# Optimization experiments

Measured on AMD Instinct MI355X. Metric: run time of the kernel, lower is better.

Reference implementation:

```python
import jax, jax.numpy as jnp
import numpy as np

T, B, M = 512, 4096, 2
DT = 1.0
HARD_RESET = True


def setup_inputs() -> dict:
    key = jax.random.key(0)
    ks = jax.random.split(key, 8)
    x_seq = jax.random.normal(ks[0], (T, B), jnp.float32) * 0.5
    w = jax.random.normal(ks[1], (B, B), jnp.float32) * (0.5 / np.sqrt(B))
    b = jax.random.normal(ks[2], (B,), jnp.float32) * 0.1
    v0 = jnp.zeros((B,), jnp.float32)
    Iasc0 = jnp.zeros((B, M), jnp.float32)
    v_th = jnp.ones((B,), jnp.float32)
    v_reset = jnp.zeros((B,), jnp.float32)
    v_rest = jnp.zeros((B,), jnp.float32)
    c_m = jnp.ones((B,), jnp.float32)
    tau = jax.random.uniform(ks[3], (B,), jnp.float32, 5.0, 20.0)
    k = jax.random.uniform(ks[4], (B, M), jnp.float32, 0.1, 0.5)
    asc = jax.random.normal(ks[5], (B, M), jnp.float32) * 0.1
    mask = jnp.ones((B,), jnp.float32)
    return dict(x_seq=x_seq, w=w, b=b, v0=v0, Iasc0=Iasc0, v_th=v_th,
                v_reset=v_reset, v_rest=v_rest, c_m=c_m, tau=tau, k=k,
                asc=asc, mask=mask)


def reference(x_seq, w, b, v0, Iasc0, v_th, v_reset, v_rest, c_m, tau, k, asc, mask):
    a = jnp.exp(-DT / tau)                 # (B,) voltage decay
    bdec = jnp.exp(-k * DT)                # (B,M) ASC decay

    def step(carry, x_t):
        v, I, s_prev = carry
        I_sum = I.sum(-1)                  # (B,)
        lin = w @ s_prev                   # recurrent GEMV against prev spikes
        x = x_t + b + lin
        v_inf = v_rest + tau * (x + I_sum) / c_m
        v_p = v_inf + (v - v_inf) * a
        u = (v_p - v_th) / (v_th - v_reset)
        s = (u > 0.0).astype(v_p.dtype) * mask
        if HARD_RESET:
            v_post = v_p - (v_p - v_reset) * s
        else:
            v_post = v_p - (v_th - v_reset) * s
        I_new = I * bdec + asc * s[:, None]
        return (v_post, I_new, s), (s, v_post)

    (v_fin, I_fin, _), (s_seq, v_seq) = jax.lax.scan(
        step, (v0, Iasc0, jnp.zeros_like(v0)), x_seq)
    return s_seq, v_seq, v_fin, I_fin
```

## Files before the change

### kernel.cpp

```cpp
#include <hip/hip_runtime.h>
#include <math.h>

#define TSTEPS 512
#define BN 4096
#define NBLK 64
#define NTHR 576
#define NPB 64
#define NGW 8
#define ESTRIDE 16

typedef unsigned long long u64;

__device__ __forceinline__ u64 ld_agent(const u64* p) {
    return __hip_atomic_load(p, __ATOMIC_RELAXED, __HIP_MEMORY_SCOPE_AGENT);
}
__device__ __forceinline__ void pub_agent(u64* p, u64 v) {
    (void)__hip_atomic_exchange(p, v, __ATOMIC_RELAXED, __HIP_MEMORY_SCOPE_AGENT);
}
__device__ __forceinline__ void st_flag(unsigned* p, unsigned v) {
    __hip_atomic_store(p, v, __ATOMIC_RELEASE, __HIP_MEMORY_SCOPE_WORKGROUP);
}
__device__ __forceinline__ unsigned ld_flag(const unsigned* p) {
    return __hip_atomic_load(p, __ATOMIC_ACQUIRE, __HIP_MEMORY_SCOPE_WORKGROUP);
}

template<bool TR>
__global__ __launch_bounds__(NTHR, 1)
void glif_kernel(const float* __restrict__ x_seq, const float* __restrict__ w,
                 const float* __restrict__ b_in, const float* __restrict__ v0,
                 const float* __restrict__ Ia0, const float* __restrict__ vth_in,
                 const float* __restrict__ vrst_in, const float* __restrict__ vrest_in,
                 const float* __restrict__ cm_in, const float* __restrict__ tau_in,
                 const float* __restrict__ k_in, const float* __restrict__ asc_in,
                 const float* __restrict__ mask_in,
                 float* __restrict__ out_s, float* __restrict__ out_v,
                 float* __restrict__ out_vf, float* __restrict__ out_if,
                 u64* __restrict__ sbuf, unsigned* __restrict__ bar,
                 float* __restrict__ wT)
{
    __shared__ float    tile[64][65];
    __shared__ int      wlist[NGW][512];
    __shared__ float4   partials[4][NGW][16];
    __shared__ unsigned flags[NGW];

    const int blk = blockIdx.x;
    const int tid = threadIdx.x;
    const int n0 = blk * NPB;
    const int wv = tid >> 6;
    const int ln = tid & 63;

    if (TR) {
        for (int tt = 0; tt < 64; ++tt) {
            int tile_id = blk + tt * NBLK;
            int ti = tile_id >> 6, tj = tile_id & 63;
            if (tid < 512) {
                int c = tid & 63, r0 = tid >> 6;
#pragma unroll
                for (int rr = 0; rr < 8; ++rr) {
                    int r = r0 + rr * 8;
                    tile[r][c] = w[(size_t)(ti * 64 + r) * BN + tj * 64 + c];
                }
            }
            __syncthreads();
            if (tid < 512) {
                int rw = tid & 63, c0 = tid >> 6;
#pragma unroll
                for (int cc = 0; cc < 8; ++cc) {
                    int cw = c0 + cc * 8;
                    float mcol = mask_in[tj * 64 + cw];
                    wT[(size_t)(tj * 64 + cw) * BN + ti * 64 + rw] = tile[rw][cw] * mcol;
                }
            }
            __syncthreads();
        }
    }

    if (tid < NGW) flags[tid] = 0;

    __syncthreads();
    if (tid == 0) {
        __threadfence();
        __hip_atomic_fetch_add(bar, 1u, __ATOMIC_ACQ_REL, __HIP_MEMORY_SCOPE_AGENT);
        while (__hip_atomic_load(bar, __ATOMIC_RELAXED, __HIP_MEMORY_SCOPE_AGENT) < NBLK) {
            __builtin_amdgcn_s_sleep(8);
        }
        __threadfence();
    }
    __syncthreads();

    if (wv == 0) {
        const int n = n0 + ln;
        float v, I0, I1, bb, aa, bd0, bd1, as0, as1, vth, vrst, vrest, cm, tau, msk;
        v = v0[n]; I0 = Ia0[2 * n]; I1 = Ia0[2 * n + 1];
        bb = b_in[n]; vth = vth_in[n]; vrst = vrst_in[n]; vrest = vrest_in[n];
        cm = cm_in[n]; tau = tau_in[n]; msk = mask_in[n];
        aa  = (float)exp((double)(-1.0f / tau));
        bd0 = (float)exp((double)(-k_in[2 * n]));
        bd1 = (float)exp((double)(-k_in[2 * n + 1]));
        as0 = asc_in[2 * n]; as1 = asc_in[2 * n + 1];

        for (int t = 0; t < TSTEPS; ++t) {
            float xt = x_seq[(size_t)t * BN + n];

            {
                const unsigned want = (unsigned)(t + 1);
                const unsigned* fp = &flags[ln & 7];
                while (ld_flag(fp) < want) {}
            }
            const float* pf = reinterpret_cast<const float*>(&partials[t & 3][0][0]);
            float l0 = pf[ln],        l1 = pf[64 + ln],  l2 = pf[128 + ln], l3 = pf[192 + ln];
            float l4 = pf[256 + ln],  l5 = pf[320 + ln], l6 = pf[384 + ln], l7 = pf[448 + ln];
            float lin = ((l0 + l1) + (l2 + l3)) + ((l4 + l5) + (l6 + l7));
            float xx = (xt + bb) + lin;
            float Isum = I0 + I1;
            float vinf = vrest + (tau * (xx + Isum)) / cm;
            float vp = vinf + (v - vinf) * aa;
            float uu = (vp - vth) / (vth - vrst);
            float s = (uu > 0.0f) ? msk : 0.0f;
            u64 bal = __ballot(s != 0.0f);
            u64 tagw = ((u64)(t + 1)) << 32;
            u64* dst = sbuf + ((size_t)((t + 1) & 1) * NBLK + blk) * ESTRIDE;
            if (ln < 2) pub_agent(dst + ln, tagw | (u64)(unsigned)(bal >> (32 * ln)));
            float vpost = vp - (vp - vrst) * s;
            I0 = I0 * bd0 + as0 * s;
            I1 = I1 * bd1 + as1 * s;
            v = vpost;
            out_s[(size_t)t * BN + n] = s;
            out_v[(size_t)t * BN + n] = vpost;
        }
        out_vf[n] = v;
        out_if[2 * n] = I0;
        out_if[2 * n + 1] = I1;
    } else {
        const int gw = wv - 1;
        const int e = ln >> 3;
        const int sub = ln & 7;
        const int wsel = sub >> 2;
        const int bshift = 8 * (sub & 3);
        const int entry = gw * 8 + e;
        const int cbase = (entry << 6) + (sub << 3);
        const int cslot = ln >> 4, l16 = ln & 15;
        const float* wb4 = wT + n0 + l16 * 4;

        for (int t = 0; t < TSTEPS; ++t) {
            const u64* p = sbuf + ((size_t)(t & 1) * NBLK + entry) * ESTRIDE + wsel;
            const unsigned want = (unsigned)t;
            u64 ev;
            for (;;) {
                u64 A = ld_agent(p);
                u64 B = ld_agent(p);
                if ((unsigned)(A >> 32) == want) { ev = A; break; }
                if ((unsigned)(B >> 32) == want) { ev = B; break; }
            }
            unsigned byte = ((unsigned)ev >> bshift) & 0xFFu;

            int c = __popc(byte);
            int x = c;
#pragma unroll
            for (int d = 1; d < 64; d <<= 1) {
                int y = __shfl_up(x, d);
                if (ln >= d) x += y;
            }
            const int kw = __shfl(x, 63);
            int base = x - c;
            while (byte) { int bp = __ffs(byte) - 1; byte &= byte - 1; wlist[gw][base++] = cbase + bp; }

            if (TR) {
                float4 acc = make_float4(0.f, 0.f, 0.f, 0.f);
                const int R = (kw + 3) >> 2;
                for (int r = 0; r < R; r += 8) {
#pragma unroll
                    for (int u = 0; u < 8; ++u) {
                        int idx = (r + u) * 4 + cslot;
                        bool pg = idx < kw;
                        int j = wlist[gw][pg ? idx : 0];
                        float m = pg ? 1.0f : 0.0f;
                        const float4 wvv = *reinterpret_cast<const float4*>(wb4 + ((size_t)j << 12));
                        acc.x = fmaf(wvv.x, m, acc.x);
                        acc.y = fmaf(wvv.y, m, acc.y);
                        acc.z = fmaf(wvv.z, m, acc.z);
                        acc.w = fmaf(wvv.w, m, acc.w);
                    }
                }
#pragma unroll
                for (int d = 16; d < 64; d <<= 1) {
                    acc.x += __shfl_xor(acc.x, d);
                    acc.y += __shfl_xor(acc.y, d);
                    acc.z += __shfl_xor(acc.z, d);
                    acc.w += __shfl_xor(acc.w, d);
                }
                if (ln < 16) partials[t & 3][gw][ln] = acc;
            } else {
                float accs = 0.f;
                const float* wrow = w + (size_t)(n0 + ln) * BN;
                for (int i = 0; i < kw; ++i) {
                    int j = wlist[gw][i];
                    accs = fmaf(wrow[j], mask_in[j], accs);
                }
                reinterpret_cast<float*>(&partials[t & 3][gw][0])[ln] = accs;
            }
            if (ln == 0) st_flag(&flags[gw], (unsigned)(t + 1));
        }
    }
}

extern "C" void kernel_launch(void* const* d_in, const int* in_sizes, int n_in,
                              void* d_out, int out_size, void* d_ws, size_t ws_size,
                              hipStream_t stream)
{
    const float* x_seq = (const float*)d_in[0];
    const float* w     = (const float*)d_in[1];
    const float* b     = (const float*)d_in[2];
    const float* v0    = (const float*)d_in[3];
    const float* Ia0   = (const float*)d_in[4];
    const float* vth   = (const float*)d_in[5];
    const float* vrst  = (const float*)d_in[6];
    const float* vrest = (const float*)d_in[7];
    const float* cm    = (const float*)d_in[8];
    const float* tau   = (const float*)d_in[9];
    const float* k     = (const float*)d_in[10];
    const float* asc   = (const float*)d_in[11];
    const float* mask  = (const float*)d_in[12];

    float* out_s  = (float*)d_out;
    float* out_v  = out_s + (size_t)TSTEPS * BN;
    float* out_vf = out_v + (size_t)TSTEPS * BN;
    float* out_if = out_vf + BN;

    const size_t mb_bytes = (size_t)2 * NBLK * ESTRIDE * sizeof(u64);
    u64* sbuf     = (u64*)d_ws;
    unsigned* bar = (unsigned*)((char*)d_ws + mb_bytes);
    float* wT     = (float*)((char*)d_ws + mb_bytes + 256);

    const size_t need = mb_bytes + 256 + (size_t)BN * BN * sizeof(float);
    const bool tr = (ws_size >= need);

    hipMemsetAsync(d_ws, 0, mb_bytes + 256, stream);

    if (tr) {
        glif_kernel<true><<<NBLK, NTHR, 0, stream>>>(
            x_seq, w, b, v0, Ia0, vth, vrst, vrest, cm, tau, k, asc, mask,
            out_s, out_v, out_vf, out_if, sbuf, bar, wT);
    } else {
        glif_kernel<false><<<NBLK, NTHR, 0, stream>>>(
            x_seq, w, b, v0, Ia0, vth, vrst, vrest, cm, tau, k, asc, mask,
            out_s, out_v, out_vf, out_if, sbuf, bar, (float*)w);
    }
}
```

Before: 1.664 ms.

## Replicate neuron state across 8 block groups and poll spike mailboxes via L2

Launches 256 blocks arranged as 8 replicas of 32 ranks, each rank owning 128 neurons. Every replica redundantly computes the full network state, so spike exchange stays within a replica group, presumably to keep mailbox traffic local to one XCD. Mailboxes are written both with a plain store and an agent-scope store, and readers poll an sc0 global load with a periodic agent-scope fallback. This trades 8x redundant GEMV and weight reads, plus a reliance on non-coherent L2 polling semantics, for lower cross-die synchronisation latency per timestep.

```diff
diff --git a/kernel.cpp b/kernel.cpp
--- a/kernel.cpp
+++ b/kernel.cpp
@@ -3,19 +3,31 @@
 
 #define TSTEPS 512
 #define BN 4096
-#define NBLK 64
+#define NBLK 256
 #define NTHR 576
-#define NPB 64
+#define NPB 128
+#define NREP 8
+#define BPR 32
+#define NWREP 128
 #define NGW 8
-#define ESTRIDE 16
+#define WPW 16
 
 typedef unsigned long long u64;
 
+__device__ __forceinline__ u64 ld_l2(const u64* p) {
+    u64 v;
+    asm volatile("global_load_dwordx2 %0, %1, off sc0\n\ts_waitcnt vmcnt(0)"
+                 : "=v"(v) : "v"(p) : "memory");
+    return v;
+}
+__device__ __forceinline__ void st_l2(u64* p, u64 v) {
+    asm volatile("global_store_dwordx2 %0, %1, off" :: "v"(p), "v"(v) : "memory");
+}
 __device__ __forceinline__ u64 ld_agent(const u64* p) {
     return __hip_atomic_load(p, __ATOMIC_RELAXED, __HIP_MEMORY_SCOPE_AGENT);
 }
-__device__ __forceinline__ void pub_agent(u64* p, u64 v) {
-    (void)__hip_atomic_exchange(p, v, __ATOMIC_RELAXED, __HIP_MEMORY_SCOPE_AGENT);
+__device__ __forceinline__ void st_agent(u64* p, u64 v) {
+    __hip_atomic_store(p, v, __ATOMIC_RELAXED, __HIP_MEMORY_SCOPE_AGENT);
 }
 __device__ __forceinline__ void st_flag(unsigned* p, unsigned v) {
     __hip_atomic_store(p, v, __ATOMIC_RELEASE, __HIP_MEMORY_SCOPE_WORKGROUP);
@@ -35,22 +47,24 @@
                  const float* __restrict__ mask_in,
                  float* __restrict__ out_s, float* __restrict__ out_v,
                  float* __restrict__ out_vf, float* __restrict__ out_if,
-                 u64* __restrict__ sbuf, unsigned* __restrict__ bar,
-                 float* __restrict__ wT)
+                 u64* __restrict__ fastmb, u64* __restrict__ fbmb,
+                 unsigned* __restrict__ bar, float* __restrict__ wT)
 {
     __shared__ float    tile[64][65];
     __shared__ int      wlist[NGW][512];
-    __shared__ float4   partials[4][NGW][16];
+    __shared__ float4   part4[4][NGW][32];
     __shared__ unsigned flags[NGW];
 
     const int blk = blockIdx.x;
     const int tid = threadIdx.x;
-    const int n0 = blk * NPB;
     const int wv = tid >> 6;
     const int ln = tid & 63;
+    const int rep = blk & 7;
+    const int rank = blk >> 3;
+    const int n0 = rank * NPB;
 
     if (TR) {
-        for (int tt = 0; tt < 64; ++tt) {
+        for (int tt = 0; tt < 16; ++tt) {
             int tile_id = blk + tt * NBLK;
             int ti = tile_id >> 6, tj = tile_id & 63;
             if (tid < 512) {
@@ -88,71 +102,110 @@
     }
     __syncthreads();
 
+    u64* fastP = fastmb + (size_t)rep * 2 * NWREP;
+    u64* fbP   = fbmb   + (size_t)rep * 2 * NWREP;
+
     if (wv == 0) {
-        const int n = n0 + ln;
-        float v, I0, I1, bb, aa, bd0, bd1, as0, as1, vth, vrst, vrest, cm, tau, msk;
-        v = v0[n]; I0 = Ia0[2 * n]; I1 = Ia0[2 * n + 1];
-        bb = b_in[n]; vth = vth_in[n]; vrst = vrst_in[n]; vrest = vrest_in[n];
-        cm = cm_in[n]; tau = tau_in[n]; msk = mask_in[n];
-        aa  = (float)exp((double)(-1.0f / tau));
-        bd0 = (float)exp((double)(-k_in[2 * n]));
-        bd1 = (float)exp((double)(-k_in[2 * n + 1]));
-        as0 = asc_in[2 * n]; as1 = asc_in[2 * n + 1];
+        const int nlo = n0 + ln, nhi = n0 + 64 + ln;
+        float vA = v0[nlo], vB = v0[nhi];
+        float I0A = Ia0[2 * nlo], I1A = Ia0[2 * nlo + 1];
+        float I0B = Ia0[2 * nhi], I1B = Ia0[2 * nhi + 1];
+        float bbA = b_in[nlo], bbB = b_in[nhi];
+        float vthA = vth_in[nlo], vthB = vth_in[nhi];
+        float vrA = vrst_in[nlo], vrB = vrst_in[nhi];
+        float veA = vrest_in[nlo], veB = vrest_in[nhi];
+        float cmA = cm_in[nlo], cmB = cm_in[nhi];
+        float tauA = tau_in[nlo], tauB = tau_in[nhi];
+        float mkA = mask_in[nlo], mkB = mask_in[nhi];
+        float aaA = (float)exp((double)(-1.0f / tauA));
+        float aaB = (float)exp((double)(-1.0f / tauB));
+        float b0A = (float)exp((double)(-k_in[2 * nlo]));
+        float b1A = (float)exp((double)(-k_in[2 * nlo + 1]));
+        float b0B = (float)exp((double)(-k_in[2 * nhi]));
+        float b1B = (float)exp((double)(-k_in[2 * nhi + 1]));
+        float s0A = asc_in[2 * nlo], s1A = asc_in[2 * nlo + 1];
+        float s0B = asc_in[2 * nhi], s1B = asc_in[2 * nhi + 1];
 
         for (int t = 0; t < TSTEPS; ++t) {
-            float xt = x_seq[(size_t)t * BN + n];
+            float xlo = x_seq[(size_t)t * BN + nlo];
+            float xhi = x_seq[(size_t)t * BN + nhi];
 
             {
                 const unsigned want = (unsigned)(t + 1);
                 const unsigned* fp = &flags[ln & 7];
                 while (ld_flag(fp) < want) {}
             }
-            const float* pf = reinterpret_cast<const float*>(&partials[t & 3][0][0]);
-            float l0 = pf[ln],        l1 = pf[64 + ln],  l2 = pf[128 + ln], l3 = pf[192 + ln];
-            float l4 = pf[256 + ln],  l5 = pf[320 + ln], l6 = pf[384 + ln], l7 = pf[448 + ln];
-            float lin = ((l0 + l1) + (l2 + l3)) + ((l4 + l5) + (l6 + l7));
-            float xx = (xt + bb) + lin;
-            float Isum = I0 + I1;
-            float vinf = vrest + (tau * (xx + Isum)) / cm;
-            float vp = vinf + (v - vinf) * aa;
-            float uu = (vp - vth) / (vth - vrst);
-            float s = (uu > 0.0f) ? msk : 0.0f;
-            u64 bal = __ballot(s != 0.0f);
-            u64 tagw = ((u64)(t + 1)) << 32;
-            u64* dst = sbuf + ((size_t)((t + 1) & 1) * NBLK + blk) * ESTRIDE;
-            if (ln < 2) pub_agent(dst + ln, tagw | (u64)(unsigned)(bal >> (32 * ln)));
-            float vpost = vp - (vp - vrst) * s;
-            I0 = I0 * bd0 + as0 * s;
-            I1 = I1 * bd1 + as1 * s;
-            v = vpost;
-            out_s[(size_t)t * BN + n] = s;
-            out_v[(size_t)t * BN + n] = vpost;
-        }
-        out_vf[n] = v;
-        out_if[2 * n] = I0;
-        out_if[2 * n + 1] = I1;
+            const float* pf = reinterpret_cast<const float*>(&part4[t & 3][0][0]);
+            float lA, lB;
+            {
+                float p0 = pf[ln],       p1 = pf[128 + ln], p2 = pf[256 + ln], p3 = pf[384 + ln];
+                float p4 = pf[512 + ln], p5 = pf[640 + ln], p6 = pf[768 + ln], p7 = pf[896 + ln];
+                lA = ((p0 + p1) + (p2 + p3)) + ((p4 + p5) + (p6 + p7));
+            }
+            {
+                int h = 64 + ln;
+                float p0 = pf[h],       p1 = pf[128 + h], p2 = pf[256 + h], p3 = pf[384 + h];
+                float p4 = pf[512 + h], p5 = pf[640 + h], p6 = pf[768 + h], p7 = pf[896 + h];
+                lB = ((p0 + p1) + (p2 + p3)) + ((p4 + p5) + (p6 + p7));
+            }
+            float xxA = (xlo + bbA) + lA;
+            float xxB = (xhi + bbB) + lB;
+            float vpA = (veA + (tauA * (xxA + (I0A + I1A))) / cmA);
+            vpA = vpA + (vA - vpA) * aaA;
+            float vpB = (veB + (tauB * (xxB + (I0B + I1B))) / cmB);
+            vpB = vpB + (vB - vpB) * aaB;
+            float sA = (((vpA - vthA) / (vthA - vrA)) > 0.0f) ? mkA : 0.0f;
+            float sB = (((vpB - vthB) / (vthB - vrB)) > 0.0f) ? mkB : 0.0f;
+            u64 bal_lo = __ballot(sA != 0.0f);
+            u64 bal_hi = __ballot(sB != 0.0f);
+            if (ln < 4) {
+                u64 bsel = (ln & 2) ? bal_hi : bal_lo;
+                unsigned pay = (ln & 1) ? (unsigned)(bsel >> 32) : (unsigned)bsel;
+                u64 ent = (((u64)(t + 1)) << 32) | (u64)pay;
+                size_t off = (size_t)((t + 1) & 1) * NWREP + rank * 4 + ln;
+                st_l2(fastP + off, ent);
+                st_agent(fbP + off, ent);
+            }
+            float voA = vpA - (vpA - vrA) * sA;
+            float voB = vpB - (vpB - vrB) * sB;
+            I0A = I0A * b0A + s0A * sA; I1A = I1A * b1A + s1A * sA;
+            I0B = I0B * b0B + s0B * sB; I1B = I1B * b1B + s1B * sB;
+            vA = voA; vB = voB;
+            if (rep == 0) {
+                out_s[(size_t)t * BN + nlo] = sA;
+                out_s[(size_t)t * BN + nhi] = sB;
+                out_v[(size_t)t * BN + nlo] = voA;
+                out_v[(size_t)t * BN + nhi] = voB;
+            }
+        }
+        if (rep == 0) {
+            out_vf[nlo] = vA; out_vf[nhi] = vB;
+            out_if[2 * nlo] = I0A; out_if[2 * nlo + 1] = I1A;
+            out_if[2 * nhi] = I0B; out_if[2 * nhi + 1] = I1B;
+        }
     } else {
         const int gw = wv - 1;
-        const int e = ln >> 3;
-        const int sub = ln & 7;
-        const int wsel = sub >> 2;
-        const int bshift = 8 * (sub & 3);
-        const int entry = gw * 8 + e;
-        const int cbase = (entry << 6) + (sub << 3);
-        const int cslot = ln >> 4, l16 = ln & 15;
-        const float* wb4 = wT + n0 + l16 * 4;
+        const int widx = gw * WPW + (ln >> 2);
+        const int sub = ln & 3;
+        const int cbase = widx * 32 + sub * 8;
+        const int cslot = ln >> 5;
+        const int r32 = ln & 31;
+        const float* wb4 = wT + n0 + r32 * 4;
 
         for (int t = 0; t < TSTEPS; ++t) {
-            const u64* p = sbuf + ((size_t)(t & 1) * NBLK + entry) * ESTRIDE + wsel;
+            const u64* pF = fastP + (size_t)(t & 1) * NWREP + widx;
+            const u64* pB = fbP   + (size_t)(t & 1) * NWREP + widx;
             const unsigned want = (unsigned)t;
-            u64 ev;
+            u64 ev; int it = 0;
             for (;;) {
-                u64 A = ld_agent(p);
-                u64 B = ld_agent(p);
+                u64 A = ld_l2(pF);
                 if ((unsigned)(A >> 32) == want) { ev = A; break; }
-                if ((unsigned)(B >> 32) == want) { ev = B; break; }
-            }
-            unsigned byte = ((unsigned)ev >> bshift) & 0xFFu;
+                if (((++it) & 7) == 0) {
+                    u64 B = ld_agent(pB);
+                    if ((unsigned)(B >> 32) == want) { ev = B; break; }
+                }
+            }
+            unsigned byte = ((unsigned)ev >> (8 * sub)) & 0xFFu;
 
             int c = __popc(byte);
             int x = c;
@@ -167,37 +220,37 @@
 
             if (TR) {
                 float4 acc = make_float4(0.f, 0.f, 0.f, 0.f);
-                const int R = (kw + 3) >> 2;
+                const int R = (kw + 1) >> 1;
                 for (int r = 0; r < R; r += 8) {
 #pragma unroll
                     for (int u = 0; u < 8; ++u) {
-                        int idx = (r + u) * 4 + cslot;
+                        int idx = (r + u) * 2 + cslot;
                         bool pg = idx < kw;
                         int j = wlist[gw][pg ? idx : 0];
                         float m = pg ? 1.0f : 0.0f;
-                        const float4 wvv = *reinterpret_cast<const float4*>(wb4 + ((size_t)j << 12));
-                        acc.x = fmaf(wvv.x, m, acc.x);
-                        acc.y = fmaf(wvv.y, m, acc.y);
-                        acc.z = fmaf(wvv.z, m, acc.z);
-                        acc.w = fmaf(wvv.w, m, acc.w);
+                        const float4 wv4 = *reinterpret_cast<const float4*>(wb4 + (size_t)j * BN);
+                        acc.x = fmaf(wv4.x, m, acc.x);
+                        acc.y = fmaf(wv4.y, m, acc.y);
+                        acc.z = fmaf(wv4.z, m, acc.z);
+                        acc.w = fmaf(wv4.w, m, acc.w);
                     }
                 }
-#pragma unroll
-                for (int d = 16; d < 64; d <<= 1) {
-                    acc.x += __shfl_xor(acc.x, d);
-                    acc.y += __shfl_xor(acc.y, d);
-                    acc.z += __shfl_xor(acc.z, d);
-                    acc.w += __shfl_xor(acc.w, d);
-                }
-                if (ln < 16) partials[t & 3][gw][ln] = acc;
+                acc.x += __shfl_xor(acc.x, 32);
+                acc.y += __shfl_xor(acc.y, 32);
+                acc.z += __shfl_xor(acc.z, 32);
+                acc.w += __shfl_xor(acc.w, 32);
+                if (ln < 32) part4[t & 3][gw][r32] = acc;
             } else {
-                float accs = 0.f;
-                const float* wrow = w + (size_t)(n0 + ln) * BN;
+                float a0 = 0.f, a1 = 0.f;
+                const float* wr0 = w + (size_t)(n0 + ln) * BN;
+                const float* wr1 = w + (size_t)(n0 + 64 + ln) * BN;
                 for (int i = 0; i < kw; ++i) {
                     int j = wlist[gw][i];
-                    accs = fmaf(wrow[j], mask_in[j], accs);
-                }
-                reinterpret_cast<float*>(&partials[t & 3][gw][0])[ln] = accs;
+                    a0 = fmaf(wr0[j], mask_in[j], a0);
+                    a1 = fmaf(wr1[j], mask_in[j], a1);
+                }
+                float* pp = reinterpret_cast<float*>(&part4[t & 3][gw][0]);
+                pp[ln] = a0; pp[64 + ln] = a1;
             }
             if (ln == 0) st_flag(&flags[gw], (unsigned)(t + 1));
         }
@@ -227,23 +280,23 @@
     float* out_vf = out_v + (size_t)TSTEPS * BN;
     float* out_if = out_vf + BN;
 
-    const size_t mb_bytes = (size_t)2 * NBLK * ESTRIDE * sizeof(u64);
-    u64* sbuf     = (u64*)d_ws;
-    unsigned* bar = (unsigned*)((char*)d_ws + mb_bytes);
-    float* wT     = (float*)((char*)d_ws + mb_bytes + 256);
-
-    const size_t need = mb_bytes + 256 + (size_t)BN * BN * sizeof(float);
+    u64* fastmb   = (u64*)d_ws;
+    u64* fbmb     = (u64*)((char*)d_ws + 16384);
+    unsigned* bar = (unsigned*)((char*)d_ws + 32768);
+    float* wT     = (float*)((char*)d_ws + 33024);
+
+    const size_t need = 33024 + (size_t)BN * BN * sizeof(float);
     const bool tr = (ws_size >= need);
 
-    hipMemsetAsync(d_ws, 0, mb_bytes + 256, stream);
+    hipMemsetAsync(d_ws, 0, 33024, stream);
 
     if (tr) {
         glif_kernel<true><<<NBLK, NTHR, 0, stream>>>(
             x_seq, w, b, v0, Ia0, vth, vrst, vrest, cm, tau, k, asc, mask,
-            out_s, out_v, out_vf, out_if, sbuf, bar, wT);
+            out_s, out_v, out_vf, out_if, fastmb, fbmb, bar, wT);
     } else {
         glif_kernel<false><<<NBLK, NTHR, 0, stream>>>(
             x_seq, w, b, v0, Ia0, vth, vrst, vrest, cm, tau, k, asc, mask,
-            out_s, out_v, out_vf, out_if, sbuf, bar, (float*)w);
+            out_s, out_v, out_vf, out_if, fastmb, fbmb, bar, (float*)w);
     }
 }
```

New measurement: 3.322 ms. 99.6% more time.
